# Performance work log

Measured on AMD Instinct MI355X. Metric: run time of the kernel, lower is better.

## Reference

```python
import jax, jax.numpy as jnp
import numpy as np

ORIG_H, ORIG_W = 256, 192
NUM_HEADS = 8
KSZ, SIGMA = 5, 2.0

def _gauss_kernel(dtype):
    off = jnp.arange(KSZ, dtype=jnp.float32) - (KSZ // 2)
    g = jnp.exp(-(off[:, None] ** 2 + off[None, :] ** 2) / (2.0 * SIGMA ** 2))
    return (g / g.sum()).astype(dtype)

def _gauss_pool(fm, kpts):
    # fm: (B,C,H,W), kpts: (B,N,2) [x,y] in original image coords -> (B,N,C)
    B, C, H, W = fm.shape
    scale = jnp.array([W / ORIG_W, H / ORIG_H], dtype=fm.dtype)
    rk = kpts * scale  # resized to feature-map coords
    off = jnp.arange(KSZ) - KSZ // 2
    ix = jnp.clip(jnp.round(rk[..., 0]).astype(jnp.int32)[..., None] + off, 0, W - 1)  # (B,N,K)
    iy = jnp.clip(jnp.round(rk[..., 1]).astype(jnp.int32)[..., None] + off, 0, H - 1)  # (B,N,K)
    fmT = fm.transpose(0, 2, 3, 1)  # (B,H,W,C)
    gather = jax.vmap(lambda f, yy, xx: f[yy[:, :, None], xx[:, None, :]])(fmT, iy, ix)  # (B,N,K,K,C)
    return jnp.einsum('bnyxc,yx->bnc', gather, _gauss_kernel(fm.dtype))

def _ln(x, g, b):
    m = x.mean(-1, keepdims=True)
    v = x.var(-1, keepdims=True)
    return (x - m) / jnp.sqrt(v + 1e-5) * g + b

def _gated_attn(x, wqkv, bqkv, wg, bg, wo, bo):
    # x: (M,S,C); headwise-gated multi-head self-attention
    M, S, C = x.shape
    H = NUM_HEADS
    d = C // H
    q, k, v = jnp.split(x @ wqkv + bqkv, 3, axis=-1)
    q = q.reshape(M, S, H, d); k = k.reshape(M, S, H, d); v = v.reshape(M, S, H, d)
    att = jax.nn.softmax(jnp.einsum('mshd,mthd->mhst', q, k) * (1.0 / np.sqrt(d)), axis=-1)
    o = jnp.einsum('mhst,mthd->mshd', att, v)
    gate = jax.nn.sigmoid(x @ wg + bg)  # (M,S,H) headwise gate
    o = (o * gate[..., None]).reshape(M, S, C)
    return o @ wo + bo

def _fuse(kf, ms, proj_p, attn_p):
    B, N, C = kf.shape
    meta = jnp.broadcast_to(ms[None], (B, N, C))
    w1, b1, g, beta, w2, b2 = proj_p
    h = _ln(jnp.concatenate([kf, meta], axis=-1) @ w1 + b1, g, beta)
    projected = jax.nn.relu(h) @ w2 + b2
    stacked = jnp.stack([kf, meta], axis=2).reshape(B * N, 2, C)  # (B*N,2,C)
    attended = _gated_attn(stacked, *attn_p).reshape(B, N, 2, C)
    return attended.mean(axis=2) + projected

def setup_inputs() -> dict:
    key = jax.random.key(0)
    ks = iter(jax.random.split(key, 48))
    B, N = 32, 17
    dims = [256, 512]
    inp = {}
    inp['fm0'] = jax.random.normal(next(ks), (B, 256, 96, 72), jnp.float32)
    inp['fm1'] = jax.random.normal(next(ks), (B, 512, 48, 36), jnp.float32)
    u = jax.random.uniform(next(ks), (B, N, 2), jnp.float32)
    inp['keypoints'] = u * jnp.array([ORIG_W - 1.0, ORIG_H - 1.0], jnp.float32)
    for i, C in enumerate(dims):
        s = 1.0 / np.sqrt(C)
        inp[f'ms{i}'] = jax.random.normal(next(ks), (N, C), jnp.float32) * s
        inp[f'p{i}_w1'] = jax.random.normal(next(ks), (2 * C, C), jnp.float32) * (1.0 / np.sqrt(2 * C))
        inp[f'p{i}_b1'] = jnp.zeros((C,), jnp.float32)
        inp[f'p{i}_g'] = jnp.ones((C,), jnp.float32)
        inp[f'p{i}_beta'] = jnp.zeros((C,), jnp.float32)
        inp[f'p{i}_w2'] = jax.random.normal(next(ks), (C, C), jnp.float32) * s
        inp[f'p{i}_b2'] = jnp.zeros((C,), jnp.float32)
        inp[f'a{i}_wqkv'] = jax.random.normal(next(ks), (C, 3 * C), jnp.float32) * s
        inp[f'a{i}_bqkv'] = jnp.zeros((3 * C,), jnp.float32)
        inp[f'a{i}_wg'] = jax.random.normal(next(ks), (C, NUM_HEADS), jnp.float32) * s
        inp[f'a{i}_bg'] = jnp.zeros((NUM_HEADS,), jnp.float32)
        inp[f'a{i}_wo'] = jax.random.normal(next(ks), (C, C), jnp.float32) * s
        inp[f'a{i}_bo'] = jnp.zeros((C,), jnp.float32)
    return inp

def reference(fm0, fm1, keypoints,
              ms0, p0_w1, p0_b1, p0_g, p0_beta, p0_w2, p0_b2,
              a0_wqkv, a0_bqkv, a0_wg, a0_bg, a0_wo, a0_bo,
              ms1, p1_w1, p1_b1, p1_g, p1_beta, p1_w2, p1_b2,
              a1_wqkv, a1_bqkv, a1_wg, a1_bg, a1_wo, a1_bo):
    kf0 = _gauss_pool(fm0, keypoints)
    f0 = _fuse(kf0, ms0, (p0_w1, p0_b1, p0_g, p0_beta, p0_w2, p0_b2),
               (a0_wqkv, a0_bqkv, a0_wg, a0_bg, a0_wo, a0_bo))
    kf1 = _gauss_pool(fm1, keypoints)
    f1 = _fuse(kf1, ms1, (p1_w1, p1_b1, p1_g, p1_beta, p1_w2, p1_b2),
               (a1_wqkv, a1_bqkv, a1_wg, a1_bg, a1_wo, a1_bo))
    return (f0, f1)
```

## Files before the change

### kernel.cpp

```cpp
#include <hip/hip_runtime.h>
#include <math.h>

#define NKPT 17
#define BATCH 32
#define MROW 544
#define MPAD 576

typedef unsigned short u16;
typedef _Float16 half8 __attribute__((ext_vector_type(8)));
typedef float f32x4 __attribute__((ext_vector_type(4)));

__device__ __forceinline__ u16 f2h(float f) {
    _Float16 h = (_Float16)f;
    u16 u; __builtin_memcpy(&u, &h, 2); return u;
}

struct GD {
    const u16* A; const u16* BT; const float* bias; float* dst;
    int lda, ldd, K, N, mstore, ntiles, sk;
};
struct GP { GD d[4]; int blk0[5]; int nd; };

__global__ __launch_bounds__(256) void gemm_fp16(GP P)
{
    __shared__ u16 sA[2][64][72];
    __shared__ u16 sB[2][64][72];
    int bid = blockIdx.x, gi = 0;
    while (gi + 1 < P.nd && bid >= P.blk0[gi + 1]) ++gi;
    const GD g = P.d[gi];
    int local = bid - P.blk0[gi];
    const int nspan = g.ntiles * g.sk;
    const int mt = local / nspan;
    int rem = local - mt * nspan;
    const int nt = rem / g.sk;
    const int s  = rem - nt * g.sk;
    const int m0 = mt * 64, n0 = nt * 64;
    const int Kseg = g.K / g.sk;
    const int kbase = s * Kseg;

    const int t = threadIdx.x;
    const int l = t & 63, w = t >> 6, wr = w >> 1, wc = w & 1;
    const int row = t >> 2, kc = (t & 3) << 4;

    f32x4 acc[2][2];
    #pragma unroll
    for (int i = 0; i < 2; ++i)
        #pragma unroll
        for (int j = 0; j < 2; ++j) { f32x4 z = {0.f,0.f,0.f,0.f}; acc[i][j] = z; }

    const u16* ap = g.A  + (size_t)(m0 + row) * g.lda + kbase + kc;
    const u16* bp = g.BT + (size_t)(n0 + row) * g.K   + kbase + kc;
    uint4 ra0 = *(const uint4*)ap, ra1 = *(const uint4*)(ap + 8);
    uint4 rb0 = *(const uint4*)bp, rb1 = *(const uint4*)(bp + 8);
    *(uint4*)&sA[0][row][kc] = ra0; *(uint4*)&sA[0][row][kc + 8] = ra1;
    *(uint4*)&sB[0][row][kc] = rb0; *(uint4*)&sB[0][row][kc + 8] = rb1;
    __syncthreads();

    int cur = 0;
    for (int k0 = 0; k0 < Kseg; k0 += 64) {
        const bool nxt = (k0 + 64 < Kseg);
        if (nxt) {
            ra0 = *(const uint4*)(ap + k0 + 64); ra1 = *(const uint4*)(ap + k0 + 72);
            rb0 = *(const uint4*)(bp + k0 + 64); rb1 = *(const uint4*)(bp + k0 + 72);
        }
        #pragma unroll
        for (int ks = 0; ks < 64; ks += 32) {
            const int koff = ks + (l >> 4) * 8;
            half8 af0 = *(const half8*)&sA[cur][wr * 32 +      (l & 15)][koff];
            half8 af1 = *(const half8*)&sA[cur][wr * 32 + 16 + (l & 15)][koff];
            half8 bf0 = *(const half8*)&sB[cur][wc * 32 +      (l & 15)][koff];
            half8 bf1 = *(const half8*)&sB[cur][wc * 32 + 16 + (l & 15)][koff];
            acc[0][0] = __builtin_amdgcn_mfma_f32_16x16x32_f16(af0, bf0, acc[0][0], 0, 0, 0);
            acc[0][1] = __builtin_amdgcn_mfma_f32_16x16x32_f16(af0, bf1, acc[0][1], 0, 0, 0);
            acc[1][0] = __builtin_amdgcn_mfma_f32_16x16x32_f16(af1, bf0, acc[1][0], 0, 0, 0);
            acc[1][1] = __builtin_amdgcn_mfma_f32_16x16x32_f16(af1, bf1, acc[1][1], 0, 0, 0);
        }
        if (nxt) {
            int nb = cur ^ 1;
            *(uint4*)&sA[nb][row][kc] = ra0; *(uint4*)&sA[nb][row][kc + 8] = ra1;
            *(uint4*)&sB[nb][row][kc] = rb0; *(uint4*)&sB[nb][row][kc + 8] = rb1;
            __syncthreads();
            cur = nb;
        }
    }

    #pragma unroll
    for (int i = 0; i < 2; ++i) {
        #pragma unroll
        for (int j = 0; j < 2; ++j) {
            int col = n0 + wc * 32 + j * 16 + (l & 15);
            float bv = (s == 0) ? g.bias[col] : 0.f;
            #pragma unroll
            for (int rr = 0; rr < 4; ++rr) {
                int m = m0 + wr * 32 + i * 16 + (l >> 4) * 4 + rr;
                if (m < g.mstore)
                    atomicAdd(&g.dst[(size_t)m * g.ldd + col], acc[i][j][rr] + bv);
            }
        }
    }
}

struct TD { const float* src; u16* dst; int K, N, blk0; };
struct PrepP {
    const float *fm0, *fm1, *kp, *ms0, *ms1;
    const float *wg0, *bg0, *wg1, *bg1;
    u16 *A1h_0, *A1h_1;
    float *gout0, *gout1;
    char* zbase;
    float* out;
    TD td[8];
};

__device__ void zero_chunk(char* base, size_t bytes, int u)
{
    size_t off = (size_t)u * 65536 + (size_t)threadIdx.x * 16;
    #pragma unroll
    for (int r = 0; r < 16; ++r) {
        size_t o = off + (size_t)r * 4096;
        if (o + 16 <= bytes) *(float4*)(base + o) = make_float4(0.f, 0.f, 0.f, 0.f);
    }
}

__device__ void gates_from_sx(const float* sx, int C, const float* wg,
                              const float* bg, float* gout8)
{
    int t = threadIdx.x;
    int h = t >> 5, e = t & 31;
    float a = 0.f;
    for (int c = e; c < C; c += 32) a += sx[c] * wg[c * 8 + h];
    a += __shfl_xor(a, 16, 32); a += __shfl_xor(a, 8, 32);
    a += __shfl_xor(a, 4, 32);  a += __shfl_xor(a, 2, 32);
    a += __shfl_xor(a, 1, 32);
    if (e == 0) gout8[h] = 1.0f / (1.0f + expf(-(a + bg[h])));
}

template<int C, int H, int W>
__device__ void pool_row(int b, int n, const float* fm, const float* kp,
                         const float* ms, u16* A1h, const float* wg,
                         const float* bg, float* gout, float* sx)
{
    const int t = threadIdx.x;
    const int e = t & 31, grp = t >> 5;
    float kx = kp[(b * NKPT + n) * 2 + 0];
    float ky = kp[(b * NKPT + n) * 2 + 1];
    int cx = (int)rintf(kx * ((float)W / 192.0f));
    int cy = (int)rintf(ky * ((float)H / 256.0f));
    int dy = e / 5, dx = e % 5;
    float wgt = 0.f; int off = 0;
    if (e < 25) {
        int iy = min(max(cy + dy - 2, 0), H - 1);
        int ix = min(max(cx + dx - 2, 0), W - 1);
        off = iy * W + ix;
        wgt = expf(-(float)((dy - 2) * (dy - 2) + (dx - 2) * (dx - 2)) / 8.0f);
    }
    float ws_ = wgt;
    ws_ += __shfl_xor(ws_, 16, 32); ws_ += __shfl_xor(ws_, 8, 32);
    ws_ += __shfl_xor(ws_, 4, 32);  ws_ += __shfl_xor(ws_, 2, 32);
    ws_ += __shfl_xor(ws_, 1, 32);
    const float inv = 1.0f / ws_;

    const size_t plane = (size_t)H * W;
    const float* pf = fm + ((size_t)b * C + grp) * plane + off;
    #pragma unroll 4
    for (int c0 = grp; c0 < C; c0 += 8, pf += 8 * plane) {
        float v = 0.f;
        if (e < 25) v = wgt * (*pf);
        v += __shfl_xor(v, 16, 32); v += __shfl_xor(v, 8, 32);
        v += __shfl_xor(v, 4, 32);  v += __shfl_xor(v, 2, 32);
        v += __shfl_xor(v, 1, 32);
        if (e == 0) sx[c0] = v * inv;
    }
    __syncthreads();
    u16* rowh = A1h + (size_t)(b * NKPT + n) * (2 * C);
    for (int c = t; c < C; c += 256) {
        rowh[c] = f2h(sx[c]);
        rowh[C + c] = f2h(ms[n * C + c]);
    }
    gates_from_sx(sx, C, wg, bg, gout + (size_t)(b * NKPT + n) * 8);
}

template<int C>
__device__ void meta_row(int n, const float* ms, u16* A1h, const float* wg,
                         const float* bg, float* gout, float* sx)
{
    const int t = threadIdx.x;
    u16* rowh = A1h + (size_t)(MROW + n) * (2 * C);
    for (int c = t; c < C; c += 256) {
        float v = ms[n * C + c];
        sx[c] = v;
        rowh[c] = f2h(v);
        rowh[C + c] = 0;
    }
    __syncthreads();
    gates_from_sx(sx, C, wg, bg, gout + (size_t)(MROW + n) * 8);
}

__device__ void wtrans_tile(const TD& d, int u, float* sT)
{
    const int ntx = d.N >> 6;
    const int tk = u / ntx, tn = u % ntx;
    const int k0 = tk << 6, n0 = tn << 6;
    const int t = threadIdx.x;
    {
        int r = t >> 2, cq = (t & 3) << 4;
        const float* sp = d.src + (size_t)(k0 + r) * d.N + n0 + cq;
        #pragma unroll
        for (int i = 0; i < 4; ++i) {
            float4 v = *(const float4*)(sp + 4 * i);
            sT[r * 65 + cq + 4 * i + 0] = v.x;
            sT[r * 65 + cq + 4 * i + 1] = v.y;
            sT[r * 65 + cq + 4 * i + 2] = v.z;
            sT[r * 65 + cq + 4 * i + 3] = v.w;
        }
    }
    __syncthreads();
    {
        int nn = t >> 2, kq = (t & 3) << 4;
        u16 hv[16] __attribute__((aligned(16)));
        #pragma unroll
        for (int i = 0; i < 16; ++i) hv[i] = f2h(sT[(kq + i) * 65 + nn]);
        u16* dp = d.dst + (size_t)(n0 + nn) * d.K + k0 + kq;
        *reinterpret_cast<uint4*>(dp) = *reinterpret_cast<uint4*>(&hv[0]);
        *reinterpret_cast<uint4*>(dp + 8) = *reinterpret_cast<uint4*>(&hv[8]);
    }
}

__global__ __launch_bounds__(256) void k1_prep(PrepP P)
{
    __shared__ float ps[64 * 65];
    int bid = blockIdx.x;
    if (bid < 1088) {
        if (bid < 544) pool_row<512, 48, 36>(bid / NKPT, bid % NKPT, P.fm1, P.kp, P.ms1, P.A1h_1, P.wg1, P.bg1, P.gout1, ps);
        else { int r = bid - 544; pool_row<256, 96, 72>(r / NKPT, r % NKPT, P.fm0, P.kp, P.ms0, P.A1h_0, P.wg0, P.bg0, P.gout0, ps); }
    } else if (bid < 1122) {
        int u = bid - 1088;
        if (u < NKPT) meta_row<512>(u, P.ms1, P.A1h_1, P.wg1, P.bg1, P.gout1, ps);
        else          meta_row<256>(u - NKPT, P.ms0, P.A1h_0, P.wg0, P.bg0, P.gout0, ps);
    } else if (bid < 1682) {
        int u = bid - 1122, i = 0;
        while (i + 1 < 8 && u >= P.td[i + 1].blk0) ++i;
        wtrans_tile(P.td[i], u - P.td[i].blk0, ps);
    } else if (bid < 1817) {
        zero_chunk(P.zbase, 8847360, bid - 1682);
    } else if (bid < 1843) {
        zero_chunk((char*)P.out, (size_t)417792 * 4, bid - 1817);
    } else if (bid == 1843) {
        zero_chunk((char*)(P.A1h_1 + (size_t)561 * 1024), 30720, 0);
    } else {
        zero_chunk((char*)(P.A1h_0 + (size_t)561 * 512), 15360, 0);
    }
}

template<int C>
__device__ void attn_row(int r, const float* qkv, const float* gout,
                         u16* om, float* sred)
{
    constexpr int D = C / 8;
    constexpr int TC = 3 * C;
    const int t = threadIdx.x;
    const int n = r % NKPT;
    const float* row  = qkv + (size_t)r * TC;
    const float* mrow = qkv + (size_t)(MROW + n) * TC;
    {
        int dot = t >> 3, sub = t & 7;
        int p = dot >> 3, h = dot & 7;
        const float* q = (p & 2) ? mrow : row;
        const float* k = ((p & 1) ? mrow : row) + C;
        float a = 0.f;
        int base = h * D + sub * (D / 8);
        #pragma unroll
        for (int i = 0; i < D / 8; ++i) a += q[base + i] * k[base + i];
        a += __shfl_xor(a, 4, 8); a += __shfl_xor(a, 2, 8); a += __shfl_xor(a, 1, 8);
        if (sub == 0) sred[dot] = a;
    }
    if (t >= 32 && t < 40) sred[32 + (t - 32)] = gout[(size_t)r * 8 + (t - 32)];
    else if (t >= 40 && t < 48) sred[32 + (t - 32)] = gout[(size_t)(MROW + n) * 8 + (t - 40)];
    __syncthreads();
    if (t < 8) {
        int h = t;
        float scale = (float)(1.0 / sqrt((double)D));
        float c0 = 0.f, c1 = 0.f;
        #pragma unroll
        for (int s = 0; s < 2; ++s) {
            float a0 = sred[(2 * s) * 8 + h] * scale;
            float a1 = sred[(2 * s + 1) * 8 + h] * scale;
            float mx = fmaxf(a0, a1);
            float e0 = expf(a0 - mx), e1 = expf(a1 - mx);
            float inv = 1.0f / (e0 + e1);
            float gt = sred[32 + s * 8 + h];
            c0 += e0 * inv * gt;
            c1 += e1 * inv * gt;
        }
        sred[48 + h] = 0.5f * c0;
        sred[56 + h] = 0.5f * c1;
    }
    __syncthreads();
    const float* v0 = row + 2 * C;
    const float* v1 = mrow + 2 * C;
    for (int c = t; c < C; c += 256) {
        int h = c / D;
        om[(size_t)r * C + c] = f2h(sred[48 + h] * v0[c] + sred[56 + h] * v1[c]);
    }
}

struct RP {
    const float *h1, *h0; u16 *h16_1, *h16_0;
    const float *g1, *be1, *g0, *be0;
    const float *qkv1, *qkv0;
    const float *gout1, *gout0;
    u16 *om1, *om0;
};
__global__ __launch_bounds__(256) void k3_rowops(RP P)
{
    __shared__ float sh[64];
    int bid = blockIdx.x;
    if (bid < 1088) {
        int lvl1 = bid < 544;
        int r = lvl1 ? bid : bid - 544;
        int C = lvl1 ? 512 : 256;
        const float* h = (lvl1 ? P.h1 : P.h0) + (size_t)r * C;
        u16* h16 = (lvl1 ? P.h16_1 : P.h16_0) + (size_t)r * C;
        const float* gg = lvl1 ? P.g1 : P.g0;
        const float* bb = lvl1 ? P.be1 : P.be0;
        int t = threadIdx.x;
        int nc = C >> 8;
        float v[2] = {0.f, 0.f};
        float s1 = 0.f, s2 = 0.f;
        for (int i = 0; i < nc; ++i) { float x = h[t + (i << 8)]; v[i] = x; s1 += x; s2 += x * x; }
        #pragma unroll
        for (int o = 32; o > 0; o >>= 1) { s1 += __shfl_down(s1, o); s2 += __shfl_down(s2, o); }
        int lane = t & 63, wv = t >> 6;
        if (lane == 0) { sh[wv * 2] = s1; sh[wv * 2 + 1] = s2; }
        __syncthreads();
        if (t == 0) {
            float a = 0.f, b = 0.f;
            #pragma unroll
            for (int q = 0; q < 4; ++q) { a += sh[q * 2]; b += sh[q * 2 + 1]; }
            float m = a / (float)C;
            float var = b / (float)C - m * m;
            sh[8] = m; sh[9] = 1.0f / sqrtf(var + 1e-5f);
        }
        __syncthreads();
        float m = sh[8], rs = sh[9];
        for (int i = 0; i < nc; ++i) {
            int c = t + (i << 8);
            float x = (v[i] - m) * rs * gg[c] + bb[c];
            h16[c] = f2h(fmaxf(x, 0.f));
        }
    } else {
        int a = bid - 1088;
        if (a < 544) attn_row<512>(a, P.qkv1, P.gout1, P.om1, sh);
        else         attn_row<256>(a - 544, P.qkv0, P.gout0, P.om0, sh);
    }
}

template<int C, int H, int W>
__global__ __launch_bounds__(C) void fb_level(
    const float* __restrict__ fm, const float* __restrict__ kp,
    const float* __restrict__ ms, const float* __restrict__ w1,
    const float* __restrict__ b1, const float* __restrict__ gvec,
    const float* __restrict__ beta, const float* __restrict__ w2,
    const float* __restrict__ b2, const float* __restrict__ wqkv,
    const float* __restrict__ bqkv, const float* __restrict__ wg,
    const float* __restrict__ bg, const float* __restrict__ wo,
    const float* __restrict__ bo, float* __restrict__ out)
{
    constexpr int D = C / 8;
    constexpr int NW = C / 64;
    __shared__ float x0[C], x1[C], hbuf[C];
    __shared__ float q0[C], k0[C], v0[C], q1[C], k1[C], v1[C];
    __shared__ float om[C];
    __shared__ float gw[25];
    __shared__ float gwsum_inv;
    __shared__ float redA[NW], redB[NW];
    __shared__ float stats[2];
    __shared__ float gates[2][8];
    __shared__ float att[2][2][8];
    const int j = threadIdx.x;
    const int blk = blockIdx.x;
    const int b = blk / NKPT, n = blk % NKPT;
    if (j < 25) { int dy = j / 5 - 2, dx = j % 5 - 2; gw[j] = expf(-(float)(dy*dy+dx*dx) / 8.0f); }
    __syncthreads();
    if (j == 0) { float s = 0.f; for (int t2 = 0; t2 < 25; ++t2) s += gw[t2]; gwsum_inv = 1.0f / s; }
    float kx = kp[(b * NKPT + n) * 2 + 0];
    float ky = kp[(b * NKPT + n) * 2 + 1];
    int cx = (int)rintf(kx * ((float)W / 192.0f));
    int cy = (int)rintf(ky * ((float)H / 256.0f));
    int ix[5], iy[5];
    #pragma unroll
    for (int t2 = 0; t2 < 5; ++t2) {
        ix[t2] = min(max(cx + t2 - 2, 0), W - 1);
        iy[t2] = min(max(cy + t2 - 2, 0), H - 1);
    }
    __syncthreads();
    {
        const float* fmb = fm + ((size_t)b * C + j) * (H * W);
        float acc = 0.f;
        #pragma unroll
        for (int yy = 0; yy < 5; ++yy) {
            const float* row = fmb + iy[yy] * W;
            #pragma unroll
            for (int xx = 0; xx < 5; ++xx) acc += gw[yy * 5 + xx] * row[ix[xx]];
        }
        x0[j] = acc * gwsum_inv;
        x1[j] = ms[n * C + j];
    }
    __syncthreads();
    float hacc = b1[j];
    for (int i = 0; i < C; ++i) hacc += x0[i] * w1[i * C + j];
    for (int i = 0; i < C; ++i) hacc += x1[i] * w1[(C + i) * C + j];
    {
        float s1 = hacc, s2 = hacc * hacc;
        #pragma unroll
        for (int o = 32; o > 0; o >>= 1) { s1 += __shfl_down(s1, o); s2 += __shfl_down(s2, o); }
        int lane = j & 63, wid = j >> 6;
        if (lane == 0) { redA[wid] = s1; redB[wid] = s2; }
        __syncthreads();
        if (j == 0) {
            float t1 = 0.f, t2 = 0.f;
            for (int w = 0; w < NW; ++w) { t1 += redA[w]; t2 += redB[w]; }
            float m = t1 / (float)C, v = t2 / (float)C - m * m;
            stats[0] = m; stats[1] = 1.0f / sqrtf(v + 1e-5f);
        }
        __syncthreads();
    }
    hbuf[j] = fmaxf((hacc - stats[0]) * stats[1] * gvec[j] + beta[j], 0.f);
    __syncthreads();
    float pj = b2[j];
    for (int i = 0; i < C; ++i) pj += hbuf[i] * w2[i * C + j];
    {
        float aq0 = bqkv[j], ak0 = bqkv[C + j], av0 = bqkv[2 * C + j];
        float aq1 = aq0, ak1 = ak0, av1 = av0;
        for (int i = 0; i < C; ++i) {
            float xi0 = x0[i], xi1 = x1[i];
            const float* wr = wqkv + (size_t)i * (3 * C);
            float wq = wr[j], wk = wr[C + j], wv = wr[2 * C + j];
            aq0 += xi0 * wq; aq1 += xi1 * wq;
            ak0 += xi0 * wk; ak1 += xi1 * wk;
            av0 += xi0 * wv; av1 += xi1 * wv;
        }
        q0[j] = aq0; k0[j] = ak0; v0[j] = av0;
        q1[j] = aq1; k1[j] = ak1; v1[j] = av1;
    }
    __syncthreads();
    if (j < 16) {
        int s = j >> 3, hh = j & 7;
        const float* xs = s ? x1 : x0;
        float a = bg[hh];
        for (int i = 0; i < C; ++i) a += xs[i] * wg[i * 8 + hh];
        gates[s][hh] = 1.0f / (1.0f + expf(-a));
    }
    if (j < 32) {
        int hh = j >> 2, st = j & 3;
        const float* qs = (st & 2) ? q1 : q0;
        const float* kt = (st & 1) ? k1 : k0;
        float a = 0.f;
        for (int i = hh * D; i < (hh + 1) * D; ++i) a += qs[i] * kt[i];
        att[(st >> 1)][st & 1][hh] = a;
    }
    __syncthreads();
    if (j < 16) {
        int s = j >> 3, hh = j & 7;
        const float inv = 1.0f / sqrtf((float)D);
        float a0 = att[s][0][hh] * inv, a1 = att[s][1][hh] * inv;
        float mx = fmaxf(a0, a1);
        float e0 = expf(a0 - mx), e1 = expf(a1 - mx);
        float den = e0 + e1;
        att[s][0][hh] = e0 / den; att[s][1][hh] = e1 / den;
    }
    __syncthreads();
    {
        int hh = j / D;
        float o0 = (att[0][0][hh] * v0[j] + att[0][1][hh] * v1[j]) * gates[0][hh];
        float o1 = (att[1][0][hh] * v0[j] + att[1][1][hh] * v1[j]) * gates[1][hh];
        om[j] = 0.5f * (o0 + o1);
    }
    __syncthreads();
    float oacc = bo[j];
    for (int i = 0; i < C; ++i) oacc += om[i] * wo[i * C + j];
    out[((size_t)b * NKPT + n) * C + j] = oacc + pj;
}

extern "C" void kernel_launch(void* const* d_in, const int* in_sizes, int n_in,
                              void* d_out, int out_size, void* d_ws, size_t ws_size,
                              hipStream_t stream) {
    (void)in_sizes; (void)n_in; (void)out_size;
    const float* fm0  = (const float*)d_in[0];
    const float* fm1  = (const float*)d_in[1];
    const float* kp   = (const float*)d_in[2];
    const float* ms0     = (const float*)d_in[3];
    const float* p0_w1   = (const float*)d_in[4];
    const float* p0_b1   = (const float*)d_in[5];
    const float* p0_g    = (const float*)d_in[6];
    const float* p0_beta = (const float*)d_in[7];
    const float* p0_w2   = (const float*)d_in[8];
    const float* p0_b2   = (const float*)d_in[9];
    const float* a0_wqkv = (const float*)d_in[10];
    const float* a0_bqkv = (const float*)d_in[11];
    const float* a0_wg   = (const float*)d_in[12];
    const float* a0_bg   = (const float*)d_in[13];
    const float* a0_wo   = (const float*)d_in[14];
    const float* a0_bo   = (const float*)d_in[15];
    const float* ms1     = (const float*)d_in[16];
    const float* p1_w1   = (const float*)d_in[17];
    const float* p1_b1   = (const float*)d_in[18];
    const float* p1_g    = (const float*)d_in[19];
    const float* p1_beta = (const float*)d_in[20];
    const float* p1_w2   = (const float*)d_in[21];
    const float* p1_b2   = (const float*)d_in[22];
    const float* a1_wqkv = (const float*)d_in[23];
    const float* a1_bqkv = (const float*)d_in[24];
    const float* a1_wg   = (const float*)d_in[25];
    const float* a1_bg   = (const float*)d_in[26];
    const float* a1_wo   = (const float*)d_in[27];
    const float* a1_bo   = (const float*)d_in[28];

    float* out0 = (float*)d_out;
    float* out1 = (float*)d_out + (size_t)MROW * 256;

    const size_t WS_NEED = 15240704;
    if (ws_size < WS_NEED || d_ws == nullptr) {
        fb_level<256, 96, 72><<<MROW, 256, 0, stream>>>(
            fm0, kp, ms0, p0_w1, p0_b1, p0_g, p0_beta, p0_w2, p0_b2,
            a0_wqkv, a0_bqkv, a0_wg, a0_bg, a0_wo, a0_bo, out0);
        fb_level<512, 48, 36><<<MROW, 512, 0, stream>>>(
            fm1, kp, ms1, p1_w1, p1_b1, p1_g, p1_beta, p1_w2, p1_b2,
            a1_wqkv, a1_bqkv, a1_wg, a1_bg, a1_wo, a1_bo, out1);
        return;
    }

    char* cur = (char*)d_ws;
    auto alloc = [&](size_t bytes) { char* p = cur; cur += (bytes + 255) & ~(size_t)255; return p; };
    u16*   A1h_1 = (u16*)alloc((size_t)MPAD * 1024 * 2);
    u16*   A1h_0 = (u16*)alloc((size_t)MPAD * 512 * 2);
    char*  zbase = cur;
    float* h_1   = (float*)alloc((size_t)MPAD * 512 * 4);
    float* h_0   = (float*)alloc((size_t)MPAD * 256 * 4);
    float* qkv_1 = (float*)alloc((size_t)MPAD * 1536 * 4);
    float* qkv_0 = (float*)alloc((size_t)MPAD * 768 * 4);
    u16*   h16_1 = (u16*)alloc((size_t)MPAD * 512 * 2);
    u16*   h16_0 = (u16*)alloc((size_t)MPAD * 256 * 2);
    u16*   om_1  = (u16*)alloc((size_t)MPAD * 512 * 2);
    u16*   om_0  = (u16*)alloc((size_t)MPAD * 256 * 2);
    u16* w1T_1   = (u16*)alloc((size_t)512 * 1024 * 2);
    u16* wqkvT_1 = (u16*)alloc((size_t)1536 * 512 * 2);
    u16* w2T_1   = (u16*)alloc((size_t)512 * 512 * 2);
    u16* woT_1   = (u16*)alloc((size_t)512 * 512 * 2);
    u16* w1T_0   = (u16*)alloc((size_t)256 * 512 * 2);
    u16* wqkvT_0 = (u16*)alloc((size_t)768 * 256 * 2);
    u16* w2T_0   = (u16*)alloc((size_t)256 * 256 * 2);
    u16* woT_0   = (u16*)alloc((size_t)256 * 256 * 2);
    float* gout1 = (float*)alloc((size_t)(MROW + NKPT) * 8 * 4);
    float* gout0 = (float*)alloc((size_t)(MROW + NKPT) * 8 * 4);

    PrepP pp;
    pp.fm0 = fm0; pp.fm1 = fm1; pp.kp = kp; pp.ms0 = ms0; pp.ms1 = ms1;
    pp.wg0 = a0_wg; pp.bg0 = a0_bg; pp.wg1 = a1_wg; pp.bg1 = a1_bg;
    pp.A1h_0 = A1h_0; pp.A1h_1 = A1h_1;
    pp.gout0 = gout0; pp.gout1 = gout1;
    pp.zbase = zbase; pp.out = (float*)d_out;
    int tcum = 0;
    auto setTD = [&](int i, const float* src, u16* dst, int K, int N) {
        pp.td[i].src = src; pp.td[i].dst = dst; pp.td[i].K = K; pp.td[i].N = N;
        pp.td[i].blk0 = tcum; tcum += (K / 64) * (N / 64);
    };
    setTD(0, p1_w1,   w1T_1,   1024, 512);
    setTD(1, a1_wqkv, wqkvT_1, 512, 1536);
    setTD(2, p1_w2,   w2T_1,   512,  512);
    setTD(3, a1_wo,   woT_1,   512,  512);
    setTD(4, p0_w1,   w1T_0,   512,  256);
    setTD(5, a0_wqkv, wqkvT_0, 256,  768);
    setTD(6, p0_w2,   w2T_0,   256,  256);
    setTD(7, a0_wo,   woT_0,   256,  256);
    k1_prep<<<1845, 256, 0, stream>>>(pp);

    GP g2; g2.nd = 4;
    g2.d[0] = { A1h_1, w1T_1,   p1_b1,   h_1,   1024, 512,  1024, 512,  MPAD, 8,  2 };
    g2.d[1] = { A1h_1, wqkvT_1, a1_bqkv, qkv_1, 1024, 1536, 512,  1536, MPAD, 24, 2 };
    g2.d[2] = { A1h_0, w1T_0,   p0_b1,   h_0,   512,  256,  512,  256,  MPAD, 4,  2 };
    g2.d[3] = { A1h_0, wqkvT_0, a0_bqkv, qkv_0, 512,  768,  256,  768,  MPAD, 12, 2 };
    g2.blk0[0] = 0;
    for (int i = 0; i < 4; ++i) g2.blk0[i + 1] = g2.blk0[i] + 9 * g2.d[i].ntiles * g2.d[i].sk;
    gemm_fp16<<<g2.blk0[4], 256, 0, stream>>>(g2);

    RP rp;
    rp.h1 = h_1; rp.h0 = h_0; rp.h16_1 = h16_1; rp.h16_0 = h16_0;
    rp.g1 = p1_g; rp.be1 = p1_beta; rp.g0 = p0_g; rp.be0 = p0_beta;
    rp.qkv1 = qkv_1; rp.qkv0 = qkv_0;
    rp.gout1 = gout1; rp.gout0 = gout0;
    rp.om1 = om_1; rp.om0 = om_0;
    k3_rowops<<<2176, 256, 0, stream>>>(rp);

    GP g4; g4.nd = 4;
    g4.d[0] = { h16_1, w2T_1, p1_b2, out1, 512, 512, 512, 512, MROW, 8, 1 };
    g4.d[1] = { om_1,  woT_1, a1_bo, out1, 512, 512, 512, 512, MROW, 8, 1 };
    g4.d[2] = { h16_0, w2T_0, p0_b2, out0, 256, 256, 256, 256, MROW, 4, 1 };
    g4.d[3] = { om_0,  woT_0, a0_bo, out0, 256, 256, 256, 256, MROW, 4, 1 };
    g4.blk0[0] = 0;
    for (int i = 0; i < 4; ++i) g4.blk0[i + 1] = g4.blk0[i] + 9 * g4.d[i].ntiles * g4.d[i].sk;
    gemm_fp16<<<g4.blk0[4], 256, 0, stream>>>(g4);
}
```

Before: 92.08 us.

## Replace atomic split-K GEMM outputs with fp16 partial buffers and fused output GEMM

The first GEMM stage now writes each split-K partial as fp16 into separate buffers, and consumers add them on read. This removes the atomicAdd accumulation and the zero-fill blocks. The two output GEMMs (w2 and wo) are merged into one K-concatenated GEMM over [relu(h) | attn_out] with pre-summed biases, written directly with plain stores using 32-row tiles. The changes cut memory traffic and atomics in exchange for fp16 rounding of the intermediate partials.

```diff
diff --git a/kernel.cpp b/kernel.cpp
--- a/kernel.cpp
+++ b/kernel.cpp
@@ -14,20 +14,23 @@
     _Float16 h = (_Float16)f;
     u16 u; __builtin_memcpy(&u, &h, 2); return u;
 }
-
-struct GD {
-    const u16* A; const u16* BT; const float* bias; float* dst;
-    int lda, ldd, K, N, mstore, ntiles, sk;
+__device__ __forceinline__ float h2f(u16 u) {
+    _Float16 h; __builtin_memcpy(&h, &u, 2); return (float)h;
+}
+
+struct GDp {
+    const u16* A; const u16* BT; const float* bias; u16* dst;
+    int lda, ldd, K, N, ntiles, sk;
 };
-struct GP { GD d[4]; int blk0[5]; int nd; };
-
-__global__ __launch_bounds__(256) void gemm_fp16(GP P)
+struct GPp { GDp d[4]; int blk0[5]; int nd; };
+
+__global__ __launch_bounds__(256) void gemm_part(GPp P)
 {
     __shared__ u16 sA[2][64][72];
     __shared__ u16 sB[2][64][72];
     int bid = blockIdx.x, gi = 0;
     while (gi + 1 < P.nd && bid >= P.blk0[gi + 1]) ++gi;
-    const GD g = P.d[gi];
+    const GDp g = P.d[gi];
     int local = bid - P.blk0[gi];
     const int nspan = g.ntiles * g.sk;
     const int mt = local / nspan;
@@ -84,6 +87,7 @@
         }
     }
 
+    u16* dbase = g.dst + (size_t)s * MPAD * g.ldd;
     #pragma unroll
     for (int i = 0; i < 2; ++i) {
         #pragma unroll
@@ -93,33 +97,93 @@
             #pragma unroll
             for (int rr = 0; rr < 4; ++rr) {
                 int m = m0 + wr * 32 + i * 16 + (l >> 4) * 4 + rr;
-                if (m < g.mstore)
-                    atomicAdd(&g.dst[(size_t)m * g.ldd + col], acc[i][j][rr] + bv);
+                dbase[(size_t)m * g.ldd + col] = f2h(acc[i][j][rr] + bv);
             }
         }
     }
 }
 
-struct TD { const float* src; u16* dst; int K, N, blk0; };
+struct GDo {
+    const u16* A; const u16* BT; const float* bias; float* dst;
+    int lda, ldd, K, N, mstore, ntiles;
+};
+struct GPo { GDo d[2]; int blk0[3]; int nd; };
+
+__global__ __launch_bounds__(256) void gemm_out(GPo P)
+{
+    __shared__ u16 sA[2][32][72];
+    __shared__ u16 sB[2][64][72];
+    int bid = blockIdx.x, gi = 0;
+    while (gi + 1 < P.nd && bid >= P.blk0[gi + 1]) ++gi;
+    const GDo g = P.d[gi];
+    int local = bid - P.blk0[gi];
+    const int mt = local / g.ntiles, nt = local % g.ntiles;
+    const int m0 = mt * 32, n0 = nt * 64;
+
+    const int t = threadIdx.x;
+    const int l = t & 63, w = t >> 6, wr = w >> 1, wc = w & 1;
+    const int rowA = t >> 3, kcA = (t & 7) << 3;
+    const int rowB = t >> 2, kcB = (t & 3) << 4;
+
+    f32x4 acc[2];
+    { f32x4 z = {0.f,0.f,0.f,0.f}; acc[0] = z; acc[1] = z; }
+
+    const u16* ap = g.A  + (size_t)(m0 + rowA) * g.lda + kcA;
+    const u16* bp = g.BT + (size_t)(n0 + rowB) * g.K   + kcB;
+    uint4 ra  = *(const uint4*)ap;
+    uint4 rb0 = *(const uint4*)bp, rb1 = *(const uint4*)(bp + 8);
+    *(uint4*)&sA[0][rowA][kcA] = ra;
+    *(uint4*)&sB[0][rowB][kcB] = rb0; *(uint4*)&sB[0][rowB][kcB + 8] = rb1;
+    __syncthreads();
+
+    int cur = 0;
+    for (int k0 = 0; k0 < g.K; k0 += 64) {
+        const bool nxt = (k0 + 64 < g.K);
+        if (nxt) {
+            ra  = *(const uint4*)(ap + k0 + 64);
+            rb0 = *(const uint4*)(bp + k0 + 64); rb1 = *(const uint4*)(bp + k0 + 72);
+        }
+        #pragma unroll
+        for (int ks = 0; ks < 64; ks += 32) {
+            const int koff = ks + (l >> 4) * 8;
+            half8 af  = *(const half8*)&sA[cur][wr * 16 + (l & 15)][koff];
+            half8 bf0 = *(const half8*)&sB[cur][wc * 32 +      (l & 15)][koff];
+            half8 bf1 = *(const half8*)&sB[cur][wc * 32 + 16 + (l & 15)][koff];
+            acc[0] = __builtin_amdgcn_mfma_f32_16x16x32_f16(af, bf0, acc[0], 0, 0, 0);
+            acc[1] = __builtin_amdgcn_mfma_f32_16x16x32_f16(af, bf1, acc[1], 0, 0, 0);
+        }
+        if (nxt) {
+            int nb = cur ^ 1;
+            *(uint4*)&sA[nb][rowA][kcA] = ra;
+            *(uint4*)&sB[nb][rowB][kcB] = rb0; *(uint4*)&sB[nb][rowB][kcB + 8] = rb1;
+            __syncthreads();
+            cur = nb;
+        }
+    }
+
+    #pragma unroll
+    for (int j = 0; j < 2; ++j) {
+        int col = n0 + wc * 32 + j * 16 + (l & 15);
+        float bv = g.bias[col];
+        #pragma unroll
+        for (int rr = 0; rr < 4; ++rr) {
+            int m = m0 + wr * 16 + (l >> 4) * 4 + rr;
+            if (m < g.mstore)
+                g.dst[(size_t)m * g.ldd + col] = acc[j][rr] + bv;
+        }
+    }
+}
+
+struct TD { const float* src; u16* dst; int K, N, ld, koff, blk0; };
 struct PrepP {
     const float *fm0, *fm1, *kp, *ms0, *ms1;
     const float *wg0, *bg0, *wg1, *bg1;
+    const float *b2_1, *bo_1, *b2_0, *bo_0;
     u16 *A1h_0, *A1h_1;
     float *gout0, *gout1;
-    char* zbase;
-    float* out;
+    float *bsum1, *bsum0;
     TD td[8];
 };
-
-__device__ void zero_chunk(char* base, size_t bytes, int u)
-{
-    size_t off = (size_t)u * 65536 + (size_t)threadIdx.x * 16;
-    #pragma unroll
-    for (int r = 0; r < 16; ++r) {
-        size_t o = off + (size_t)r * 4096;
-        if (o + 16 <= bytes) *(float4*)(base + o) = make_float4(0.f, 0.f, 0.f, 0.f);
-    }
-}
 
 __device__ void gates_from_sx(const float* sx, int C, const float* wg,
                               const float* bg, float* gout8)
@@ -219,7 +283,7 @@
         u16 hv[16] __attribute__((aligned(16)));
         #pragma unroll
         for (int i = 0; i < 16; ++i) hv[i] = f2h(sT[(kq + i) * 65 + nn]);
-        u16* dp = d.dst + (size_t)(n0 + nn) * d.K + k0 + kq;
+        u16* dp = d.dst + (size_t)(n0 + nn) * d.ld + d.koff + k0 + kq;
         *reinterpret_cast<uint4*>(dp) = *reinterpret_cast<uint4*>(&hv[0]);
         *reinterpret_cast<uint4*>(dp + 8) = *reinterpret_cast<uint4*>(&hv[8]);
     }
@@ -240,36 +304,36 @@
         int u = bid - 1122, i = 0;
         while (i + 1 < 8 && u >= P.td[i + 1].blk0) ++i;
         wtrans_tile(P.td[i], u - P.td[i].blk0, ps);
-    } else if (bid < 1817) {
-        zero_chunk(P.zbase, 8847360, bid - 1682);
-    } else if (bid < 1843) {
-        zero_chunk((char*)P.out, (size_t)417792 * 4, bid - 1817);
-    } else if (bid == 1843) {
-        zero_chunk((char*)(P.A1h_1 + (size_t)561 * 1024), 30720, 0);
     } else {
-        zero_chunk((char*)(P.A1h_0 + (size_t)561 * 512), 15360, 0);
+        int t = threadIdx.x;
+        for (int c = t; c < 512; c += 256) P.bsum1[c] = P.b2_1[c] + P.bo_1[c];
+        for (int c = t; c < 256; c += 256) P.bsum0[c] = P.b2_0[c] + P.bo_0[c];
     }
 }
 
 template<int C>
-__device__ void attn_row(int r, const float* qkv, const float* gout,
-                         u16* om, float* sred)
+__device__ void attn_row(int r, const u16* qkvp, const float* gout,
+                         u16* A4, float* sred)
 {
     constexpr int D = C / 8;
     constexpr int TC = 3 * C;
+    const size_t PS = (size_t)MPAD * TC;
     const int t = threadIdx.x;
     const int n = r % NKPT;
-    const float* row  = qkv + (size_t)r * TC;
-    const float* mrow = qkv + (size_t)(MROW + n) * TC;
+    const size_t rb = (size_t)r * TC;
+    const size_t mb = (size_t)(MROW + n) * TC;
     {
         int dot = t >> 3, sub = t & 7;
         int p = dot >> 3, h = dot & 7;
-        const float* q = (p & 2) ? mrow : row;
-        const float* k = ((p & 1) ? mrow : row) + C;
+        size_t qb = ((p & 2) ? mb : rb) + h * D + sub * (D / 8);
+        size_t kb = ((p & 1) ? mb : rb) + C + h * D + sub * (D / 8);
         float a = 0.f;
-        int base = h * D + sub * (D / 8);
-        #pragma unroll
-        for (int i = 0; i < D / 8; ++i) a += q[base + i] * k[base + i];
+        #pragma unroll
+        for (int i = 0; i < D / 8; ++i) {
+            float qv = h2f(qkvp[qb + i]) + h2f(qkvp[qb + i + PS]);
+            float kv = h2f(qkvp[kb + i]) + h2f(qkvp[kb + i + PS]);
+            a += qv * kv;
+        }
         a += __shfl_xor(a, 4, 8); a += __shfl_xor(a, 2, 8); a += __shfl_xor(a, 1, 8);
         if (sub == 0) sred[dot] = a;
     }
@@ -295,20 +359,20 @@
         sred[56 + h] = 0.5f * c1;
     }
     __syncthreads();
-    const float* v0 = row + 2 * C;
-    const float* v1 = mrow + 2 * C;
     for (int c = t; c < C; c += 256) {
         int h = c / D;
-        om[(size_t)r * C + c] = f2h(sred[48 + h] * v0[c] + sred[56 + h] * v1[c]);
+        float v0 = h2f(qkvp[rb + 2 * C + c]) + h2f(qkvp[rb + 2 * C + c + PS]);
+        float v1 = h2f(qkvp[mb + 2 * C + c]) + h2f(qkvp[mb + 2 * C + c + PS]);
+        A4[(size_t)r * (2 * C) + C + c] = f2h(sred[48 + h] * v0 + sred[56 + h] * v1);
     }
 }
 
 struct RP {
-    const float *h1, *h0; u16 *h16_1, *h16_0;
+    const u16 *hp1, *hp0;
+    u16 *A4_1, *A4_0;
     const float *g1, *be1, *g0, *be0;
-    const float *qkv1, *qkv0;
+    const u16 *qkvp1, *qkvp0;
     const float *gout1, *gout0;
-    u16 *om1, *om0;
 };
 __global__ __launch_bounds__(256) void k3_rowops(RP P)
 {
@@ -318,15 +382,20 @@
         int lvl1 = bid < 544;
         int r = lvl1 ? bid : bid - 544;
         int C = lvl1 ? 512 : 256;
-        const float* h = (lvl1 ? P.h1 : P.h0) + (size_t)r * C;
-        u16* h16 = (lvl1 ? P.h16_1 : P.h16_0) + (size_t)r * C;
+        const u16* hp = lvl1 ? P.hp1 : P.hp0;
+        const size_t PSh = (size_t)MPAD * C;
+        u16* A4 = (lvl1 ? P.A4_1 : P.A4_0) + (size_t)r * (2 * C);
         const float* gg = lvl1 ? P.g1 : P.g0;
         const float* bb = lvl1 ? P.be1 : P.be0;
         int t = threadIdx.x;
         int nc = C >> 8;
         float v[2] = {0.f, 0.f};
         float s1 = 0.f, s2 = 0.f;
-        for (int i = 0; i < nc; ++i) { float x = h[t + (i << 8)]; v[i] = x; s1 += x; s2 += x * x; }
+        for (int i = 0; i < nc; ++i) {
+            size_t idx = (size_t)r * C + t + (i << 8);
+            float x = h2f(hp[idx]) + h2f(hp[idx + PSh]);
+            v[i] = x; s1 += x; s2 += x * x;
+        }
         #pragma unroll
         for (int o = 32; o > 0; o >>= 1) { s1 += __shfl_down(s1, o); s2 += __shfl_down(s2, o); }
         int lane = t & 63, wv = t >> 6;
@@ -345,12 +414,12 @@
         for (int i = 0; i < nc; ++i) {
             int c = t + (i << 8);
             float x = (v[i] - m) * rs * gg[c] + bb[c];
-            h16[c] = f2h(fmaxf(x, 0.f));
+            A4[c] = f2h(fmaxf(x, 0.f));
         }
     } else {
         int a = bid - 1088;
-        if (a < 544) attn_row<512>(a, P.qkv1, P.gout1, P.om1, sh);
-        else         attn_row<256>(a - 544, P.qkv0, P.gout0, P.om0, sh);
+        if (a < 544) attn_row<512>(a, P.qkvp1, P.gout1, P.A4_1, sh);
+        else         attn_row<256>(a - 544, P.qkvp0, P.gout0, P.A4_0, sh);
     }
 }
 
@@ -518,7 +587,7 @@
     float* out0 = (float*)d_out;
     float* out1 = (float*)d_out + (size_t)MROW * 256;
 
-    const size_t WS_NEED = 15240704;
+    const size_t WS_NEED = 15400000;
     if (ws_size < WS_NEED || d_ws == nullptr) {
         fb_level<256, 96, 72><<<MROW, 256, 0, stream>>>(
             fm0, kp, ms0, p0_w1, p0_b1, p0_g, p0_beta, p0_w2, p0_b2,
@@ -531,72 +600,68 @@
 
     char* cur = (char*)d_ws;
     auto alloc = [&](size_t bytes) { char* p = cur; cur += (bytes + 255) & ~(size_t)255; return p; };
-    u16*   A1h_1 = (u16*)alloc((size_t)MPAD * 1024 * 2);
-    u16*   A1h_0 = (u16*)alloc((size_t)MPAD * 512 * 2);
-    char*  zbase = cur;
-    float* h_1   = (float*)alloc((size_t)MPAD * 512 * 4);
-    float* h_0   = (float*)alloc((size_t)MPAD * 256 * 4);
-    float* qkv_1 = (float*)alloc((size_t)MPAD * 1536 * 4);
-    float* qkv_0 = (float*)alloc((size_t)MPAD * 768 * 4);
-    u16*   h16_1 = (u16*)alloc((size_t)MPAD * 512 * 2);
-    u16*   h16_0 = (u16*)alloc((size_t)MPAD * 256 * 2);
-    u16*   om_1  = (u16*)alloc((size_t)MPAD * 512 * 2);
-    u16*   om_0  = (u16*)alloc((size_t)MPAD * 256 * 2);
+    u16* A1h_1 = (u16*)alloc((size_t)MPAD * 1024 * 2);
+    u16* A1h_0 = (u16*)alloc((size_t)MPAD * 512 * 2);
+    u16* hp_1  = (u16*)alloc((size_t)2 * MPAD * 512 * 2);
+    u16* hp_0  = (u16*)alloc((size_t)2 * MPAD * 256 * 2);
+    u16* qkvp_1 = (u16*)alloc((size_t)2 * MPAD * 1536 * 2);
+    u16* qkvp_0 = (u16*)alloc((size_t)2 * MPAD * 768 * 2);
+    u16* A4_1  = (u16*)alloc((size_t)MPAD * 1024 * 2);
+    u16* A4_0  = (u16*)alloc((size_t)MPAD * 512 * 2);
     u16* w1T_1   = (u16*)alloc((size_t)512 * 1024 * 2);
     u16* wqkvT_1 = (u16*)alloc((size_t)1536 * 512 * 2);
-    u16* w2T_1   = (u16*)alloc((size_t)512 * 512 * 2);
-    u16* woT_1   = (u16*)alloc((size_t)512 * 512 * 2);
+    u16* w24T_1  = (u16*)alloc((size_t)512 * 1024 * 2);
     u16* w1T_0   = (u16*)alloc((size_t)256 * 512 * 2);
     u16* wqkvT_0 = (u16*)alloc((size_t)768 * 256 * 2);
-    u16* w2T_0   = (u16*)alloc((size_t)256 * 256 * 2);
-    u16* woT_0   = (u16*)alloc((size_t)256 * 256 * 2);
+    u16* w24T_0  = (u16*)alloc((size_t)256 * 512 * 2);
     float* gout1 = (float*)alloc((size_t)(MROW + NKPT) * 8 * 4);
     float* gout0 = (float*)alloc((size_t)(MROW + NKPT) * 8 * 4);
+    float* bsum1 = (float*)alloc(512 * 4);
+    float* bsum0 = (float*)alloc(256 * 4);
 
     PrepP pp;
     pp.fm0 = fm0; pp.fm1 = fm1; pp.kp = kp; pp.ms0 = ms0; pp.ms1 = ms1;
     pp.wg0 = a0_wg; pp.bg0 = a0_bg; pp.wg1 = a1_wg; pp.bg1 = a1_bg;
+    pp.b2_1 = p1_b2; pp.bo_1 = a1_bo; pp.b2_0 = p0_b2; pp.bo_0 = a0_bo;
     pp.A1h_0 = A1h_0; pp.A1h_1 = A1h_1;
     pp.gout0 = gout0; pp.gout1 = gout1;
-    pp.zbase = zbase; pp.out = (float*)d_out;
+    pp.bsum1 = bsum1; pp.bsum0 = bsum0;
     int tcum = 0;
-    auto setTD = [&](int i, const float* src, u16* dst, int K, int N) {
+    auto setTD = [&](int i, const float* src, u16* dst, int K, int N, int ld, int koff) {
         pp.td[i].src = src; pp.td[i].dst = dst; pp.td[i].K = K; pp.td[i].N = N;
+        pp.td[i].ld = ld; pp.td[i].koff = koff;
         pp.td[i].blk0 = tcum; tcum += (K / 64) * (N / 64);
     };
-    setTD(0, p1_w1,   w1T_1,   1024, 512);
-    setTD(1, a1_wqkv, wqkvT_1, 512, 1536);
-    setTD(2, p1_w2,   w2T_1,   512,  512);
-    setTD(3, a1_wo,   woT_1,   512,  512);
-    setTD(4, p0_w1,   w1T_0,   512,  256);
-    setTD(5, a0_wqkv, wqkvT_0, 256,  768);
-    setTD(6, p0_w2,   w2T_0,   256,  256);
-    setTD(7, a0_wo,   woT_0,   256,  256);
-    k1_prep<<<1845, 256, 0, stream>>>(pp);
-
-    GP g2; g2.nd = 4;
-    g2.d[0] = { A1h_1, w1T_1,   p1_b1,   h_1,   1024, 512,  1024, 512,  MPAD, 8,  2 };
-    g2.d[1] = { A1h_1, wqkvT_1, a1_bqkv, qkv_1, 1024, 1536, 512,  1536, MPAD, 24, 2 };
-    g2.d[2] = { A1h_0, w1T_0,   p0_b1,   h_0,   512,  256,  512,  256,  MPAD, 4,  2 };
-    g2.d[3] = { A1h_0, wqkvT_0, a0_bqkv, qkv_0, 512,  768,  256,  768,  MPAD, 12, 2 };
+    setTD(0, p1_w1,   w1T_1,   1024, 512,  1024, 0);
+    setTD(1, a1_wqkv, wqkvT_1, 512,  1536, 512,  0);
+    setTD(2, p1_w2,   w24T_1,  512,  512,  1024, 0);
+    setTD(3, a1_wo,   w24T_1,  512,  512,  1024, 512);
+    setTD(4, p0_w1,   w1T_0,   512,  256,  512,  0);
+    setTD(5, a0_wqkv, wqkvT_0, 256,  768,  256,  0);
+    setTD(6, p0_w2,   w24T_0,  256,  256,  512,  0);
+    setTD(7, a0_wo,   w24T_0,  256,  256,  512,  256);
+    k1_prep<<<1683, 256, 0, stream>>>(pp);
+
+    GPp g2; g2.nd = 4;
+    g2.d[0] = { A1h_1, w1T_1,   p1_b1,   hp_1,   1024, 512,  1024, 512,  8,  2 };
+    g2.d[1] = { A1h_1, wqkvT_1, a1_bqkv, qkvp_1, 1024, 1536, 512,  1536, 24, 2 };
+    g2.d[2] = { A1h_0, w1T_0,   p0_b1,   hp_0,   512,  256,  512,  256,  4,  2 };
+    g2.d[3] = { A1h_0, wqkvT_0, a0_bqkv, qkvp_0, 512,  768,  256,  768,  12, 2 };
     g2.blk0[0] = 0;
     for (int i = 0; i < 4; ++i) g2.blk0[i + 1] = g2.blk0[i] + 9 * g2.d[i].ntiles * g2.d[i].sk;
-    gemm_fp16<<<g2.blk0[4], 256, 0, stream>>>(g2);
+    gemm_part<<<g2.blk0[4], 256, 0, stream>>>(g2);
 
     RP rp;
-    rp.h1 = h_1; rp.h0 = h_0; rp.h16_1 = h16_1; rp.h16_0 = h16_0;
+    rp.hp1 = hp_1; rp.hp0 = hp_0; rp.A4_1 = A4_1; rp.A4_0 = A4_0;
     rp.g1 = p1_g; rp.be1 = p1_beta; rp.g0 = p0_g; rp.be0 = p0_beta;
-    rp.qkv1 = qkv_1; rp.qkv0 = qkv_0;
+    rp.qkvp1 = qkvp_1; rp.qkvp0 = qkvp_0;
     rp.gout1 = gout1; rp.gout0 = gout0;
-    rp.om1 = om_1; rp.om0 = om_0;
     k3_rowops<<<2176, 256, 0, stream>>>(rp);
 
-    GP g4; g4.nd = 4;
-    g4.d[0] = { h16_1, w2T_1, p1_b2, out1, 512, 512, 512, 512, MROW, 8, 1 };
-    g4.d[1] = { om_1,  woT_1, a1_bo, out1, 512, 512, 512, 512, MROW, 8, 1 };
-    g4.d[2] = { h16_0, w2T_0, p0_b2, out0, 256, 256, 256, 256, MROW, 4, 1 };
-    g4.d[3] = { om_0,  woT_0, a0_bo, out0, 256, 256, 256, 256, MROW, 4, 1 };
+    GPo g4; g4.nd = 2;
+    g4.d[0] = { A4_1, w24T_1, bsum1, out1, 1024, 512, 1024, 512, MROW, 8 };
+    g4.d[1] = { A4_0, w24T_0, bsum0, out0, 512,  256, 512,  256, MROW, 4 };
     g4.blk0[0] = 0;
-    for (int i = 0; i < 4; ++i) g4.blk0[i + 1] = g4.blk0[i] + 9 * g4.d[i].ntiles * g4.d[i].sk;
-    gemm_fp16<<<g4.blk0[4], 256, 0, stream>>>(g4);
-}
+    for (int i = 0; i < 2; ++i) g4.blk0[i + 1] = g4.blk0[i] + 18 * g4.d[i].ntiles;
+    gemm_out<<<g4.blk0[2], 256, 0, stream>>>(g4);
+}
```

After: 82.30 us, median of 2. -10.6%, faster.
